# Performance work log

Hardware: AMD Instinct MI355X
Metric: run time of the kernel (lower is better)

## Reference

```python
import jax, jax.numpy as jnp
import numpy as np

NUM_HEADS = 16
ROPE_BASE = 10000.0
QK_GAIN_INIT = 12.0
EPS = 1e-6
# head_config = alternating ['rope','nope',...]; 1.0 -> RoPE applied to this head
ROPE_MASK = jnp.asarray(np.tile([1.0, 0.0], NUM_HEADS // 2), dtype=jnp.float32)


def setup_inputs() -> dict:
    key = jax.random.key(0)
    k0, k1, k2 = jax.random.split(key, 3)
    B, S, Dm = 2, 2048, 2048
    x = jax.random.normal(k0, (B, S, Dm), dtype=jnp.float32)
    # fused QKV projection and output projection (out_proj flagged zero-init in the
    # original; we use small random init so outputs/grads are non-trivial)
    w_qkv = jax.random.normal(k1, (Dm, 3 * Dm), dtype=jnp.float32) * (Dm ** -0.5)
    w_out = jax.random.normal(k2, (Dm, Dm), dtype=jnp.float32) * (Dm ** -0.5)
    q_gain = jnp.full((NUM_HEADS,), QK_GAIN_INIT, dtype=jnp.float32)
    return {"x": x, "w_qkv": w_qkv, "w_out": w_out, "q_gain": q_gain}


def _rope_cos_sin(seqlen, head_dim, dtype):
    half = head_dim // 2
    inv_freq = ROPE_BASE ** (-jnp.arange(0, half, dtype=jnp.float32) / half)
    theta = jnp.arange(seqlen, dtype=jnp.float32)[:, None] * inv_freq[None, :]  # [S, D/2]
    return jnp.cos(theta).astype(dtype), jnp.sin(theta).astype(dtype)


def _apply_rope(t, cos, sin):
    # t: [B, S, H, D]; cos/sin: [S, D/2] -> broadcast [1, S, 1, D/2]
    d2 = t.shape[-1] // 2
    t1, t2 = t[..., :d2], t[..., d2:]
    c = cos[None, :, None, :]
    s = sin[None, :, None, :]
    return jnp.concatenate([t1 * c - t2 * s, t1 * s + t2 * c], axis=-1)


def _unit_norm(t):
    # per-head-dim L2 normalization (qk-norm)
    return t * jax.lax.rsqrt(jnp.sum(t * t, axis=-1, keepdims=True) + EPS)


def reference(x, w_qkv, w_out, q_gain):
    B, S, Dm = x.shape
    H = NUM_HEADS
    D = Dm // H
    qkv = (x @ w_qkv).reshape(B, S, 3, H, D)
    q, k, v = qkv[:, :, 0], qkv[:, :, 1], qkv[:, :, 2]  # [B, S, H, D]
    q = _unit_norm(q)
    k = _unit_norm(k)
    cos, sin = _rope_cos_sin(S, D, x.dtype)
    m = ROPE_MASK[None, None, :, None]  # heterogeneous per-head dispatch
    q = m * _apply_rope(q, cos, sin) + (1.0 - m) * q
    k = m * _apply_rope(k, cos, sin) + (1.0 - m) * k
    # per-head learned qk gain instead of 1/sqrt(d)
    logits = jnp.einsum('bshd,bthd->bhst', q, k) * q_gain[None, :, None, None]
    causal = jnp.tril(jnp.ones((S, S), dtype=bool))
    logits = jnp.where(causal[None, None], logits, jnp.finfo(logits.dtype).min)
    attn = jax.nn.softmax(logits, axis=-1)
    y = jnp.einsum('bhst,bthd->bshd', attn, v).reshape(B, S, Dm)
    return y @ w_out
```

## Files before the change

### kernel.cpp

```cpp
#include <hip/hip_runtime.h>
#include <hip/hip_bf16.h>

typedef unsigned short ushort_t;
typedef __attribute__((ext_vector_type(8))) short short8;
typedef __attribute__((ext_vector_type(4))) float floatx4;

#define B_  2
#define S_  2048
#define DM_ 2048
#define H_  16
#define DH_ 128

#define AS1(p) ((const __attribute__((address_space(1))) void*)(p))
#define AS3(p) ((__attribute__((address_space(3))) void*)(p))

static __device__ __forceinline__ float b2f(ushort_t u) {
  __hip_bfloat16 h = *reinterpret_cast<__hip_bfloat16*>(&u);
  return __bfloat162float(h);
}
static __device__ __forceinline__ ushort_t f2b(float f) {
  __hip_bfloat16 h = __float2bfloat16(f);
  return *reinterpret_cast<ushort_t*>(&h);
}
static __device__ __forceinline__ float fast_exp2(float x) {
#if defined(__has_builtin)
#if __has_builtin(__builtin_amdgcn_exp2f)
  return __builtin_amdgcn_exp2f(x);
#else
  return exp2f(x);
#endif
#else
  return exp2f(x);
#endif
}

__global__ __launch_bounds__(256) void convert_f32_bf16(const float* __restrict__ in,
                                                        ushort_t* __restrict__ out) {
  size_t i = ((size_t)blockIdx.x * 256 + threadIdx.x) * 8;
  float4 a = *(const float4*)(in + i);
  float4 b = *(const float4*)(in + i + 4);
  ushort_t tmp[8] = {f2b(a.x), f2b(a.y), f2b(a.z), f2b(a.w),
                     f2b(b.x), f2b(b.y), f2b(b.z), f2b(b.w)};
  *(uint4*)(out + i) = *(const uint4*)tmp;
}

__global__ __launch_bounds__(256) void transpose_f32_to_bf16T(const float* __restrict__ in,
                                                              ushort_t* __restrict__ out,
                                                              int R, int inC, int colOff) {
  __shared__ ushort_t tile[64][72];
  const int tid = threadIdx.x;
  const int r0 = blockIdx.y * 64, c0 = blockIdx.x * 64;
#pragma unroll
  for (int p = 0; p < 2; ++p) {
    int li = tid + p * 256;
    int r = li >> 3, cs = (li & 7) * 8;
    const float* src = in + (size_t)(r0 + r) * inC + colOff + c0 + cs;
    float4 a = *(const float4*)src;
    float4 b = *(const float4*)(src + 4);
    ushort_t tmp[8] = {f2b(a.x), f2b(a.y), f2b(a.z), f2b(a.w),
                       f2b(b.x), f2b(b.y), f2b(b.z), f2b(b.w)};
    *(uint4*)&tile[r][cs] = *(const uint4*)tmp;
  }
  __syncthreads();
#pragma unroll
  for (int p = 0; p < 2; ++p) {
    int li = tid + p * 256;
    int cR = li >> 3, rs = (li & 7) * 8;
    ushort_t tmp[8];
#pragma unroll
    for (int e = 0; e < 8; ++e) tmp[e] = tile[rs + e][cR];
    *(uint4*)(out + (size_t)(c0 + cR) * R + r0 + rs) = *(const uint4*)tmp;
  }
}

template <int MODE>
__global__ __launch_bounds__(256) void gemm_bt_async(const ushort_t* __restrict__ A,
                                                     const ushort_t* __restrict__ Bt,
                                                     void* __restrict__ C0,
                                                     void* __restrict__ C1,
                                                     int M, int N, int K) {
  __shared__ alignas(16) ushort_t As[2][128 * 32];
  __shared__ alignas(16) ushort_t Bs[2][128 * 32];
  const int tid = threadIdx.x;
  const int wave = tid >> 6, lane = tid & 63;
  const int l15 = lane & 15, quad = lane >> 4;
  const int wr = (wave >> 1) * 64, wc = (wave & 1) * 64;
  const int lin = blockIdx.y * gridDim.x + blockIdx.x;
  const int band = lin / (4 * gridDim.x);
  const int rin = lin % (4 * gridDim.x);
  const int by = band * 4 + (rin & 3);
  const int bx = rin >> 2;
  const size_t m0 = (size_t)by * 128, n0 = (size_t)bx * 128;
  const int srow = lane >> 2, scol = (lane & 3) * 8;

  floatx4 zero = {0.f, 0.f, 0.f, 0.f};
  floatx4 acc[4][4];
#pragma unroll
  for (int i = 0; i < 4; ++i)
#pragma unroll
    for (int j = 0; j < 4; ++j) acc[i][j] = zero;

  auto stage = [&](int kt, int bf) {
#pragma unroll
    for (int i = 0; i < 2; ++i) {
      int c = wave * 2 + i;
      int row = c * 16 + srow;
      __builtin_amdgcn_global_load_lds(AS1(A + (m0 + row) * K + kt + scol),
                                       AS3((char*)As[bf] + c * 1024), 16, 0, 0);
      __builtin_amdgcn_global_load_lds(AS1(Bt + (n0 + row) * K + kt + scol),
                                       AS3((char*)Bs[bf] + c * 1024), 16, 0, 0);
    }
  };

  stage(0, 0);
  const int niter = K / 32;
  for (int it = 0; it < niter; ++it) {
    const int cur = it & 1;
    __syncthreads();
    if (it + 1 < niter) stage((it + 1) * 32, cur ^ 1);

    short8 af[4], bfr[4];
#pragma unroll
    for (int i = 0; i < 4; ++i)
      af[i] = *(const short8*)&As[cur][(wr + i * 16 + l15) * 32 + quad * 8];
#pragma unroll
    for (int j = 0; j < 4; ++j)
      bfr[j] = *(const short8*)&Bs[cur][(wc + j * 16 + l15) * 32 + quad * 8];
#pragma unroll
    for (int i = 0; i < 4; ++i)
#pragma unroll
      for (int j = 0; j < 4; ++j)
        acc[i][j] = __builtin_amdgcn_mfma_f32_16x16x32_bf16(af[i], bfr[j], acc[i][j], 0, 0, 0);
  }

#pragma unroll
  for (int i = 0; i < 4; ++i)
#pragma unroll
    for (int j = 0; j < 4; ++j)
#pragma unroll
      for (int r = 0; r < 4; ++r) {
        size_t row = m0 + wr + i * 16 + quad * 4 + r;
        size_t col = n0 + wc + j * 16 + l15;
        if (MODE == 1)
          ((float*)C0)[row * N + col] = acc[i][j][r];
        else
          ((ushort_t*)C0)[row * N + col] = f2b(acc[i][j][r]);
      }
}

#define SBAR() __builtin_amdgcn_sched_barrier(0)
#define BARR() __builtin_amdgcn_s_barrier()

#define LDS_A(qm, bb)                                                          \
  _Pragma("unroll") for (int mi = 0; mi < 4; ++mi) {                           \
    _Pragma("unroll") for (int ks = 0; ks < 2; ++ks) {                         \
      const int r_ = arow + (qm) * 64 + mi * 16;                               \
      const int cb_ = ((ks) * 64 + quad * 16) ^ swz;                           \
      afr[qm][mi][ks] =                                                        \
          *(const short8*)((const char*)As[bb] + r_ * 128 + cb_);              \
    }                                                                          \
  }

#define LDS_B(qn, bb)                                                          \
  _Pragma("unroll") for (int ni = 0; ni < 2; ++ni) {                           \
    _Pragma("unroll") for (int ks = 0; ks < 2; ++ks) {                         \
      const int r_ = brow + (qn) * 32 + ni * 16;                               \
      const int cb_ = ((ks) * 64 + quad * 16) ^ swz;                           \
      bfr[qn][ni][ks] =                                                        \
          *(const short8*)((const char*)Bs[bb] + r_ * 128 + cb_);              \
    }                                                                          \
  }

#define MMA_Q(qm, qn)                                                          \
  _Pragma("unroll") for (int mi = 0; mi < 4; ++mi) {                           \
    _Pragma("unroll") for (int ni = 0; ni < 2; ++ni) {                         \
      floatx4 t_ = acc[(qm) * 4 + mi][(qn) * 2 + ni];                          \
      t_ = __builtin_amdgcn_mfma_f32_16x16x32_bf16(afr[qm][mi][0],             \
                                                   bfr[qn][ni][0], t_, 0, 0, 0); \
      t_ = __builtin_amdgcn_mfma_f32_16x16x32_bf16(afr[qm][mi][1],             \
                                                   bfr[qn][ni][1], t_, 0, 0, 0); \
      acc[(qm) * 4 + mi][(qn) * 2 + ni] = t_;                                  \
    }                                                                          \
  }

template <int MODE>
__global__ __launch_bounds__(512, 2) void gemm_bt_256(const ushort_t* __restrict__ A,
                                                      const ushort_t* __restrict__ Bt,
                                                      void* __restrict__ C0,
                                                      void* __restrict__ C1,
                                                      int M, int N, int K) {
  __shared__ alignas(16) ushort_t As[2][256 * 64];
  __shared__ alignas(16) ushort_t Bs[2][256 * 64];
  const int tid = threadIdx.x;
  const int wave = tid >> 6, lane = tid & 63;
  const int l15 = lane & 15, quad = lane >> 4;
  const int wm = wave >> 2, wn = wave & 3;
  const size_t m0 = (size_t)blockIdx.y * 256, n0 = (size_t)blockIdx.x * 256;
  const int nkt = K >> 6;

  const int srow = lane >> 3;
  const int skk = ((lane & 7) ^ srow) * 8;

  const int arow = wm * 128 + l15;
  const int brow = wn * 64 + l15;
  const int swz = (l15 & 7) << 4;

  floatx4 zero = {0.f, 0.f, 0.f, 0.f};
  floatx4 acc[8][4];
#pragma unroll
  for (int i = 0; i < 8; ++i)
#pragma unroll
    for (int j = 0; j < 4; ++j) acc[i][j] = zero;

  short8 afr[2][4][2];
  short8 bfr[2][2][2];

  auto stage_half = [&](int t, int ht) {
    if (t >= nkt) return;
    const int bb = t & 1;
    const int h = ht & 1;
    const int kt64 = t << 6;
    const ushort_t* G = (ht < 2) ? A : Bt;
    const size_t r0 = (ht < 2) ? m0 : n0;
    char* dst = (char*)((ht < 2) ? As[bb] : Bs[bb]) + h * 16384;
#pragma unroll
    for (int i = 0; i < 2; ++i) {
      const int c = wave * 2 + i;
      const size_t gr = r0 + h * 128 + c * 8 + srow;
      __builtin_amdgcn_global_load_lds(AS1(G + gr * K + kt64 + skk),
                                       AS3(dst + c * 1024), 16, 0, 0);
    }
  };

  stage_half(0, 0); stage_half(0, 1); stage_half(0, 2); stage_half(0, 3);
  stage_half(1, 0); stage_half(1, 1); stage_half(1, 2); stage_half(1, 3);
  SBAR();
  if (nkt > 1) { asm volatile("s_waitcnt vmcnt(8)" ::: "memory"); }
  else         { asm volatile("s_waitcnt vmcnt(0)" ::: "memory"); }
  SBAR(); BARR(); SBAR();

  for (int kt = 0; kt < nkt; ++kt) {
    const int bb = kt & 1;
    LDS_A(0, bb); LDS_B(0, bb);
    SBAR(); BARR(); SBAR();
    __builtin_amdgcn_s_setprio(1);
    MMA_Q(0, 0);
    __builtin_amdgcn_s_setprio(0);
    SBAR(); BARR(); SBAR();
    LDS_A(1, bb);
    SBAR(); BARR(); SBAR();
    __builtin_amdgcn_s_setprio(1);
    MMA_Q(1, 0);
    __builtin_amdgcn_s_setprio(0);
    SBAR(); BARR(); SBAR();
    LDS_B(1, bb);
    stage_half(kt + 2, 0); stage_half(kt + 2, 1);
    SBAR(); BARR(); SBAR();
    __builtin_amdgcn_s_setprio(1);
    MMA_Q(1, 1);
    __builtin_amdgcn_s_setprio(0);
    SBAR(); BARR(); SBAR();
    stage_half(kt + 2, 2); stage_half(kt + 2, 3);
    SBAR(); BARR(); SBAR();
    __builtin_amdgcn_s_setprio(1);
    MMA_Q(0, 1);
    __builtin_amdgcn_s_setprio(0);
    SBAR();
    if (kt + 2 < nkt) { asm volatile("s_waitcnt vmcnt(8)" ::: "memory"); }
    else              { asm volatile("s_waitcnt vmcnt(0)" ::: "memory"); }
    SBAR(); BARR(); SBAR();
  }

  if (MODE == 2) {
    ushort_t* Cb = (n0 >= 2048) ? (ushort_t*)C1 : (ushort_t*)C0;
    size_t nc0 = n0 & 2047;
#pragma unroll
    for (int mi8 = 0; mi8 < 8; ++mi8)
#pragma unroll
      for (int nj = 0; nj < 4; ++nj)
#pragma unroll
        for (int r = 0; r < 4; ++r) {
          size_t row = m0 + wm * 128 + (mi8 >> 2) * 64 + (mi8 & 3) * 16 + quad * 4 + r;
          size_t col = nc0 + wn * 64 + (nj >> 1) * 32 + (nj & 1) * 16 + l15;
          Cb[row * 2048 + col] = f2b(acc[mi8][nj][r]);
        }
  } else {
#pragma unroll
    for (int mi8 = 0; mi8 < 8; ++mi8)
#pragma unroll
      for (int nj = 0; nj < 4; ++nj)
#pragma unroll
        for (int r = 0; r < 4; ++r) {
          size_t row = m0 + wm * 128 + (mi8 >> 2) * 64 + (mi8 & 3) * 16 + quad * 4 + r;
          size_t col = n0 + wn * 64 + (nj >> 1) * 32 + (nj & 1) * 16 + l15;
          if (MODE == 1)
            ((float*)C0)[row * N + col] = acc[mi8][nj][r];
          else
            ((ushort_t*)C0)[row * N + col] = f2b(acc[mi8][nj][r]);
        }
  }
}

__global__ __launch_bounds__(256) void norm_rope(ushort_t* __restrict__ Q,
                                                 ushort_t* __restrict__ Kb,
                                                 const float* __restrict__ gain) {
  const int tid = threadIdx.x;
  const int wave = tid >> 6, lane = tid & 63;
  const int g16 = lane >> 4, sl = lane & 15;
  const int idx = (blockIdx.x * 4 + wave) * 4 + g16;
  const int h = idx & 15;
  const int s = (idx >> 4) & (S_ - 1);
  const size_t off = (size_t)(idx >> 4) * DM_ + h * DH_ + sl * 4;

  ushort_t qv1[4], qv2[4], kv1[4], kv2[4];
  *(uint2*)qv1 = *(const uint2*)(Q + off);
  *(uint2*)qv2 = *(const uint2*)(Q + off + 64);
  *(uint2*)kv1 = *(const uint2*)(Kb + off);
  *(uint2*)kv2 = *(const uint2*)(Kb + off + 64);

  float q1[4], q2[4], k1[4], k2[4];
  float sq = 0.f, sk = 0.f;
#pragma unroll
  for (int e = 0; e < 4; ++e) {
    q1[e] = b2f(qv1[e]); q2[e] = b2f(qv2[e]);
    k1[e] = b2f(kv1[e]); k2[e] = b2f(kv2[e]);
    sq += q1[e] * q1[e] + q2[e] * q2[e];
    sk += k1[e] * k1[e] + k2[e] * k2[e];
  }
#pragma unroll
  for (int o = 1; o < 16; o <<= 1) {
    sq += __shfl_xor(sq, o, 64);
    sk += __shfl_xor(sk, o, 64);
  }
  float rq = rsqrtf(sq + 1e-6f), rk = rsqrtf(sk + 1e-6f);
  const float g = gain[h] * 1.44269504f;
  const bool roped = (h & 1) == 0;
#pragma unroll
  for (int e = 0; e < 4; ++e) {
    float a = q1[e] * rq, bq = q2[e] * rq;
    float c_ = k1[e] * rk, dk = k2[e] * rk;
    if (roped) {
      int j = sl * 4 + e;
      float invf = exp2f((float)j * -0.20762050593f);
      float th = (float)s * invf;
      float cc = cosf(th), sn = sinf(th);
      float na = a * cc - bq * sn, nb = a * sn + bq * cc;
      float nc = c_ * cc - dk * sn, nd = c_ * sn + dk * cc;
      a = na; bq = nb; c_ = nc; dk = nd;
    }
    qv1[e] = f2b(a * g); qv2[e] = f2b(bq * g);
    kv1[e] = f2b(c_);    kv2[e] = f2b(dk);
  }
  *(uint2*)(Q + off)       = *(const uint2*)qv1;
  *(uint2*)(Q + off + 64)  = *(const uint2*)qv2;
  *(uint2*)(Kb + off)      = *(const uint2*)kv1;
  *(uint2*)(Kb + off + 64) = *(const uint2*)kv2;
}

__global__ __launch_bounds__(256, 2) void attn(ushort_t* __restrict__ QY,
                                               const ushort_t* __restrict__ Kg,
                                               const ushort_t* __restrict__ Vg) {
  __shared__ alignas(16) ushort_t Ks[2][64 * 128];
  __shared__ alignas(16) ushort_t Vs[2][128 * 64];
  __shared__ alignas(16) ushort_t Ps[2][4][16 * 64];

  const float M0 = 18.755035531f;
  const int tid = threadIdx.x;
  const int wave = tid >> 6, lane = tid & 63;
  const int l15 = lane & 15, quad = lane >> 4;
  const int bh = blockIdx.x;
  const int b = bh >> 4, h = bh & 15;
  const int p = blockIdx.y;
  const int qt[2] = {p, 31 - p};

  const ushort_t* Kgb = Kg + (size_t)b * S_ * DM_ + h * DH_;
  const ushort_t* Vgb = Vg + (size_t)(h * DH_) * (B_ * S_) + b * S_;

  short8 aq[2][4];
#pragma unroll
  for (int t = 0; t < 2; ++t) {
    const ushort_t* Qg =
        QY + (size_t)(b * S_ + qt[t] * 64 + wave * 16 + l15) * DM_ + h * DH_;
#pragma unroll
    for (int ks = 0; ks < 4; ++ks)
      aq[t][ks] = *(const short8*)(Qg + ks * 32 + quad * 8);
  }

  float lsum[2][4] = {{0.f, 0.f, 0.f, 0.f}, {0.f, 0.f, 0.f, 0.f}};
  floatx4 zero = {0.f, 0.f, 0.f, 0.f};
  floatx4 oacc[2][8];
#pragma unroll
  for (int t = 0; t < 2; ++t)
#pragma unroll
    for (int d = 0; d < 8; ++d) oacc[t][d] = zero;

  const int krow_in = lane >> 4, ksd = lane & 15;
  const int vrow_in = lane >> 3, vsd = lane & 7;

  auto stage = [&](int kt, int bf) {
#pragma unroll
    for (int i = 0; i < 4; ++i) {
      int c = wave * 4 + i;
      {
        int r = c * 4 + krow_in;
        int sg = ksd ^ (r & 7);
        __builtin_amdgcn_global_load_lds(
            AS1(Kgb + (size_t)(kt * 64 + r) * DM_ + sg * 8),
            AS3((char*)Ks[bf] + c * 1024), 16, 0, 0);
      }
      {
        int r = c * 8 + vrow_in;
        int sg = vsd ^ (r & 7);
        __builtin_amdgcn_global_load_lds(
            AS1(Vgb + (size_t)r * (B_ * S_) + kt * 64 + sg * 8),
            AS3((char*)Vs[bf] + c * 1024), 16, 0, 0);
      }
    }
  };

  stage(0, 0);

  for (int kt = 0; kt <= qt[1]; ++kt) {
    const int cur = kt & 1;
    __syncthreads();
    if (kt < qt[1]) stage(kt + 1, cur ^ 1);

#pragma unroll
    for (int t = 0; t < 2; ++t) {
      if (t == 0 && kt > qt[0]) continue;
      floatx4 sacc[4];
#pragma unroll
      for (int j = 0; j < 4; ++j) sacc[j] = zero;
#pragma unroll
      for (int ks = 0; ks < 4; ++ks) {
#pragma unroll
        for (int j = 0; j < 4; ++j) {
          int row = j * 16 + l15;
          int sl = (ks * 4 + quad) ^ (row & 7);
          short8 bk = *(const short8*)&Ks[cur][row * 128 + sl * 8];
          sacc[j] = __builtin_amdgcn_mfma_f32_16x16x32_bf16(aq[t][ks], bk, sacc[j], 0, 0, 0);
        }
      }
      if (kt == qt[t]) {
#pragma unroll
        for (int j = 0; j < 4; ++j)
#pragma unroll
          for (int r = 0; r < 4; ++r) {
            int key = j * 16 + l15;
            int qr = wave * 16 + quad * 4 + r;
            if (key > qr) sacc[j][r] = -1e30f;
          }
      }
#pragma unroll
      for (int j = 0; j < 4; ++j)
#pragma unroll
        for (int r = 0; r < 4; ++r) {
          float pv = fast_exp2(sacc[j][r] - M0);
          sacc[j][r] = pv;
          lsum[t][r] += pv;
        }
#pragma unroll
      for (int j = 0; j < 4; ++j)
#pragma unroll
        for (int r = 0; r < 4; ++r) {
          int row = quad * 4 + r;
          int col = j * 16 + l15;
          int g = col >> 3, w = col & 7;
          Ps[t][wave][row * 64 + ((g ^ (row & 7)) << 3) + w] = f2b(sacc[j][r]);
        }
#pragma unroll
      for (int ks2 = 0; ks2 < 2; ++ks2) {
        short8 ap = *(const short8*)&Ps[t][wave][l15 * 64 +
                                                (((ks2 * 4 + quad) ^ (l15 & 7)) << 3)];
#pragma unroll
        for (int d = 0; d < 8; ++d) {
          int row = d * 16 + l15;
          int sl = (ks2 * 4 + quad) ^ (row & 7);
          short8 bv = *(const short8*)&Vs[cur][row * 64 + sl * 8];
          oacc[t][d] = __builtin_amdgcn_mfma_f32_16x16x32_bf16(ap, bv, oacc[t][d], 0, 0, 0);
        }
      }
    }
  }

#pragma unroll
  for (int t = 0; t < 2; ++t) {
#pragma unroll
    for (int r = 0; r < 4; ++r) {
#pragma unroll
      for (int o = 1; o < 16; o <<= 1) lsum[t][r] += __shfl_xor(lsum[t][r], o, 64);
      float inv = 1.0f / lsum[t][r];
      size_t row = (size_t)(b * S_ + qt[t] * 64 + wave * 16 + quad * 4 + r);
#pragma unroll
      for (int d = 0; d < 8; ++d) {
        size_t col = (size_t)h * DH_ + d * 16 + l15;
        QY[row * DM_ + col] = f2b(oacc[t][d][r] * inv);
      }
    }
  }
}

extern "C" void kernel_launch(void* const* d_in, const int* in_sizes, int n_in,
                              void* d_out, int out_size, void* d_ws, size_t ws_size,
                              hipStream_t stream) {
  const float* x      = (const float*)d_in[0];
  const float* w_qkv  = (const float*)d_in[1];
  const float* w_out  = (const float*)d_in[2];
  const float* q_gain = (const float*)d_in[3];
  float* out = (float*)d_out;

  char* ws = (char*)d_ws;
  const size_t bsd = (size_t)B_ * S_ * DM_;
  ushort_t* Qraw = (ushort_t*)ws;
  ushort_t* Kraw = Qraw + bsd;
  ushort_t* Vt   = Kraw + bsd;
  ushort_t* wvT  = Vt + bsd;
  ushort_t* xbf  = (ushort_t*)d_out;
  ushort_t* wqkT = xbf + bsd;
  ushort_t* woutT = Kraw;

  convert_f32_bf16<<<dim3(bsd / (8 * 256)), 256, 0, stream>>>(x, xbf);
  transpose_f32_to_bf16T<<<dim3(64, 32), 256, 0, stream>>>(w_qkv, wqkT, DM_, 3 * DM_, 0);
  transpose_f32_to_bf16T<<<dim3(32, 32), 256, 0, stream>>>(w_qkv, wvT, DM_, 3 * DM_, 2 * DM_);

  gemm_bt_256<2><<<dim3(16, 16), 512, 0, stream>>>(xbf, wqkT, Qraw, Kraw,
                                                   B_ * S_, 2 * DM_, DM_);
  gemm_bt_async<0><<<dim3(32, 16), 256, 0, stream>>>(wvT, xbf, Vt, nullptr,
                                                     DM_, B_ * S_, DM_);
  norm_rope<<<dim3(B_ * S_ * H_ / 16), 256, 0, stream>>>(Qraw, Kraw, q_gain);
  attn<<<dim3(B_ * H_, S_ / 128), 256, 0, stream>>>(Qraw, Kraw, Vt);
  transpose_f32_to_bf16T<<<dim3(32, 32), 256, 0, stream>>>(w_out, woutT, DM_, DM_, 0);
  gemm_bt_async<1><<<dim3(16, 32), 256, 0, stream>>>(Qraw, woutT, out, nullptr,
                                                     B_ * S_, DM_, DM_);
}
```

Measured before the change: 372.7 us.

## Replace simple 128x128 GEMM with swizzled, phase-pipelined kernel; rebalance 256 GEMM prefetch

Replaces the simple double-buffered 128x128 K=32 GEMM used for the V projection and output projection with a new K=64 kernel. The new kernel uses XOR-swizzled LDS, quarter-tile async loads interleaved between MFMA phases, barriers with setprio, and two blocks per CU. The existing 256 GEMM's prefetch schedule is also changed to issue loads one iteration ahead in smaller pieces, with a lower vmcnt wait threshold. The aim is to overlap global loads with MFMA work and cut LDS bank conflicts. The cost is more barriers per iteration, and the shallower in-flight load depth in the 256 GEMM could expose latency.

Result: faster. 363.8 us (-2.4%).

```diff
diff --git a/kernel.cpp b/kernel.cpp
--- a/kernel.cpp
+++ b/kernel.cpp
@@ -71,81 +71,6 @@
     for (int e = 0; e < 8; ++e) tmp[e] = tile[rs + e][cR];
     *(uint4*)(out + (size_t)(c0 + cR) * R + r0 + rs) = *(const uint4*)tmp;
   }
-}
-
-template <int MODE>
-__global__ __launch_bounds__(256) void gemm_bt_async(const ushort_t* __restrict__ A,
-                                                     const ushort_t* __restrict__ Bt,
-                                                     void* __restrict__ C0,
-                                                     void* __restrict__ C1,
-                                                     int M, int N, int K) {
-  __shared__ alignas(16) ushort_t As[2][128 * 32];
-  __shared__ alignas(16) ushort_t Bs[2][128 * 32];
-  const int tid = threadIdx.x;
-  const int wave = tid >> 6, lane = tid & 63;
-  const int l15 = lane & 15, quad = lane >> 4;
-  const int wr = (wave >> 1) * 64, wc = (wave & 1) * 64;
-  const int lin = blockIdx.y * gridDim.x + blockIdx.x;
-  const int band = lin / (4 * gridDim.x);
-  const int rin = lin % (4 * gridDim.x);
-  const int by = band * 4 + (rin & 3);
-  const int bx = rin >> 2;
-  const size_t m0 = (size_t)by * 128, n0 = (size_t)bx * 128;
-  const int srow = lane >> 2, scol = (lane & 3) * 8;
-
-  floatx4 zero = {0.f, 0.f, 0.f, 0.f};
-  floatx4 acc[4][4];
-#pragma unroll
-  for (int i = 0; i < 4; ++i)
-#pragma unroll
-    for (int j = 0; j < 4; ++j) acc[i][j] = zero;
-
-  auto stage = [&](int kt, int bf) {
-#pragma unroll
-    for (int i = 0; i < 2; ++i) {
-      int c = wave * 2 + i;
-      int row = c * 16 + srow;
-      __builtin_amdgcn_global_load_lds(AS1(A + (m0 + row) * K + kt + scol),
-                                       AS3((char*)As[bf] + c * 1024), 16, 0, 0);
-      __builtin_amdgcn_global_load_lds(AS1(Bt + (n0 + row) * K + kt + scol),
-                                       AS3((char*)Bs[bf] + c * 1024), 16, 0, 0);
-    }
-  };
-
-  stage(0, 0);
-  const int niter = K / 32;
-  for (int it = 0; it < niter; ++it) {
-    const int cur = it & 1;
-    __syncthreads();
-    if (it + 1 < niter) stage((it + 1) * 32, cur ^ 1);
-
-    short8 af[4], bfr[4];
-#pragma unroll
-    for (int i = 0; i < 4; ++i)
-      af[i] = *(const short8*)&As[cur][(wr + i * 16 + l15) * 32 + quad * 8];
-#pragma unroll
-    for (int j = 0; j < 4; ++j)
-      bfr[j] = *(const short8*)&Bs[cur][(wc + j * 16 + l15) * 32 + quad * 8];
-#pragma unroll
-    for (int i = 0; i < 4; ++i)
-#pragma unroll
-      for (int j = 0; j < 4; ++j)
-        acc[i][j] = __builtin_amdgcn_mfma_f32_16x16x32_bf16(af[i], bfr[j], acc[i][j], 0, 0, 0);
-  }
-
-#pragma unroll
-  for (int i = 0; i < 4; ++i)
-#pragma unroll
-    for (int j = 0; j < 4; ++j)
-#pragma unroll
-      for (int r = 0; r < 4; ++r) {
-        size_t row = m0 + wr + i * 16 + quad * 4 + r;
-        size_t col = n0 + wc + j * 16 + l15;
-        if (MODE == 1)
-          ((float*)C0)[row * N + col] = acc[i][j][r];
-        else
-          ((ushort_t*)C0)[row * N + col] = f2b(acc[i][j][r]);
-      }
 }
 
 #define SBAR() __builtin_amdgcn_sched_barrier(0)
@@ -233,40 +158,42 @@
   };
 
   stage_half(0, 0); stage_half(0, 1); stage_half(0, 2); stage_half(0, 3);
-  stage_half(1, 0); stage_half(1, 1); stage_half(1, 2); stage_half(1, 3);
+  stage_half(1, 0); stage_half(1, 1);
   SBAR();
-  if (nkt > 1) { asm volatile("s_waitcnt vmcnt(8)" ::: "memory"); }
+  if (nkt > 1) { asm volatile("s_waitcnt vmcnt(4)" ::: "memory"); }
   else         { asm volatile("s_waitcnt vmcnt(0)" ::: "memory"); }
   SBAR(); BARR(); SBAR();
 
   for (int kt = 0; kt < nkt; ++kt) {
     const int bb = kt & 1;
     LDS_A(0, bb); LDS_B(0, bb);
+    stage_half(kt + 1, 2);
     SBAR(); BARR(); SBAR();
     __builtin_amdgcn_s_setprio(1);
     MMA_Q(0, 0);
     __builtin_amdgcn_s_setprio(0);
     SBAR(); BARR(); SBAR();
     LDS_A(1, bb);
+    stage_half(kt + 1, 3);
     SBAR(); BARR(); SBAR();
     __builtin_amdgcn_s_setprio(1);
     MMA_Q(1, 0);
     __builtin_amdgcn_s_setprio(0);
     SBAR(); BARR(); SBAR();
     LDS_B(1, bb);
-    stage_half(kt + 2, 0); stage_half(kt + 2, 1);
+    stage_half(kt + 2, 0);
     SBAR(); BARR(); SBAR();
     __builtin_amdgcn_s_setprio(1);
     MMA_Q(1, 1);
     __builtin_amdgcn_s_setprio(0);
     SBAR(); BARR(); SBAR();
-    stage_half(kt + 2, 2); stage_half(kt + 2, 3);
+    stage_half(kt + 2, 1);
     SBAR(); BARR(); SBAR();
     __builtin_amdgcn_s_setprio(1);
     MMA_Q(0, 1);
     __builtin_amdgcn_s_setprio(0);
     SBAR();
-    if (kt + 2 < nkt) { asm volatile("s_waitcnt vmcnt(8)" ::: "memory"); }
+    if (kt + 2 < nkt) { asm volatile("s_waitcnt vmcnt(4)" ::: "memory"); }
     else              { asm volatile("s_waitcnt vmcnt(0)" ::: "memory"); }
     SBAR(); BARR(); SBAR();
   }
@@ -299,6 +226,147 @@
             ((ushort_t*)C0)[row * N + col] = f2b(acc[mi8][nj][r]);
         }
   }
+}
+
+#define LDS_A8(mh, bb)                                                         \
+  _Pragma("unroll") for (int mi = 0; mi < 2; ++mi) {                           \
+    _Pragma("unroll") for (int ks = 0; ks < 2; ++ks) {                         \
+      const int r_ = arow + ((mh) * 2 + mi) * 16;                              \
+      const int cb_ = ((ks) * 64 + quad * 16) ^ swz;                           \
+      afr[(mh) * 2 + mi][ks] =                                                 \
+          *(const short8*)((const char*)As[bb] + r_ * 128 + cb_);              \
+    }                                                                          \
+  }
+
+#define LDS_B8(nh, bb)                                                         \
+  _Pragma("unroll") for (int ni = 0; ni < 2; ++ni) {                           \
+    _Pragma("unroll") for (int ks = 0; ks < 2; ++ks) {                         \
+      const int r_ = brow + ((nh) * 2 + ni) * 16;                              \
+      const int cb_ = ((ks) * 64 + quad * 16) ^ swz;                           \
+      bfr[(nh) * 2 + ni][ks] =                                                 \
+          *(const short8*)((const char*)Bs[bb] + r_ * 128 + cb_);              \
+    }                                                                          \
+  }
+
+#define MMA_H(mh, nh)                                                          \
+  _Pragma("unroll") for (int mi = 0; mi < 2; ++mi) {                           \
+    _Pragma("unroll") for (int ni = 0; ni < 2; ++ni) {                         \
+      floatx4 t_ = acc[(mh) * 2 + mi][(nh) * 2 + ni];                          \
+      t_ = __builtin_amdgcn_mfma_f32_16x16x32_bf16(afr[(mh) * 2 + mi][0],      \
+                                                   bfr[(nh) * 2 + ni][0], t_, 0, 0, 0); \
+      t_ = __builtin_amdgcn_mfma_f32_16x16x32_bf16(afr[(mh) * 2 + mi][1],      \
+                                                   bfr[(nh) * 2 + ni][1], t_, 0, 0, 0); \
+      acc[(mh) * 2 + mi][(nh) * 2 + ni] = t_;                                  \
+    }                                                                          \
+  }
+
+template <int MODE>
+__global__ __launch_bounds__(256, 2) void gemm_bt_128(const ushort_t* __restrict__ A,
+                                                      const ushort_t* __restrict__ Bt,
+                                                      void* __restrict__ C0,
+                                                      int M, int N, int K) {
+  __shared__ alignas(16) ushort_t As[2][128 * 64];
+  __shared__ alignas(16) ushort_t Bs[2][128 * 64];
+  const int tid = threadIdx.x;
+  const int wave = tid >> 6, lane = tid & 63;
+  const int l15 = lane & 15, quad = lane >> 4;
+  const int wm = wave >> 1, wn = wave & 1;
+  const int lin = blockIdx.y * gridDim.x + blockIdx.x;
+  const int band = lin / (4 * gridDim.x);
+  const int rin = lin % (4 * gridDim.x);
+  const int by = band * 4 + (rin & 3);
+  const int bx = rin >> 2;
+  const size_t m0 = (size_t)by * 128, n0 = (size_t)bx * 128;
+  const int nkt = K >> 6;
+
+  const int srow = lane >> 3;
+  const int skk = ((lane & 7) ^ srow) * 8;
+
+  const int arow = wm * 64 + l15;
+  const int brow = wn * 64 + l15;
+  const int swz = (l15 & 7) << 4;
+
+  floatx4 zero = {0.f, 0.f, 0.f, 0.f};
+  floatx4 acc[4][4];
+#pragma unroll
+  for (int i = 0; i < 4; ++i)
+#pragma unroll
+    for (int j = 0; j < 4; ++j) acc[i][j] = zero;
+
+  short8 afr[4][2];
+  short8 bfr[4][2];
+
+  auto stage_q = [&](int t, int qt_) {
+    if (t >= nkt) return;
+    const int bb = t & 1;
+    const int h = qt_ & 1;
+    const int kt64 = t << 6;
+    const ushort_t* G = (qt_ < 2) ? A : Bt;
+    const size_t r0 = (qt_ < 2) ? m0 : n0;
+    char* dst = (char*)((qt_ < 2) ? As[bb] : Bs[bb]) + h * 8192;
+#pragma unroll
+    for (int i = 0; i < 2; ++i) {
+      const int c = wave * 2 + i;
+      const size_t gr = r0 + h * 64 + c * 8 + srow;
+      __builtin_amdgcn_global_load_lds(AS1(G + gr * K + kt64 + skk),
+                                       AS3(dst + c * 1024), 16, 0, 0);
+    }
+  };
+
+  stage_q(0, 0); stage_q(0, 1); stage_q(0, 2); stage_q(0, 3);
+  stage_q(1, 0); stage_q(1, 1);
+  SBAR();
+  if (nkt > 1) { asm volatile("s_waitcnt vmcnt(4)" ::: "memory"); }
+  else         { asm volatile("s_waitcnt vmcnt(0)" ::: "memory"); }
+  SBAR(); BARR(); SBAR();
+
+  for (int kt = 0; kt < nkt; ++kt) {
+    const int bb = kt & 1;
+    LDS_A8(0, bb); LDS_B8(0, bb);
+    stage_q(kt + 1, 2);
+    SBAR(); BARR(); SBAR();
+    __builtin_amdgcn_s_setprio(1);
+    MMA_H(0, 0);
+    __builtin_amdgcn_s_setprio(0);
+    SBAR(); BARR(); SBAR();
+    LDS_A8(1, bb);
+    stage_q(kt + 1, 3);
+    SBAR(); BARR(); SBAR();
+    __builtin_amdgcn_s_setprio(1);
+    MMA_H(1, 0);
+    __builtin_amdgcn_s_setprio(0);
+    SBAR(); BARR(); SBAR();
+    LDS_B8(1, bb);
+    stage_q(kt + 2, 0);
+    SBAR(); BARR(); SBAR();
+    __builtin_amdgcn_s_setprio(1);
+    MMA_H(1, 1);
+    __builtin_amdgcn_s_setprio(0);
+    SBAR(); BARR(); SBAR();
+    stage_q(kt + 2, 1);
+    SBAR(); BARR(); SBAR();
+    __builtin_amdgcn_s_setprio(1);
+    MMA_H(0, 1);
+    __builtin_amdgcn_s_setprio(0);
+    SBAR();
+    if (kt + 2 < nkt) { asm volatile("s_waitcnt vmcnt(4)" ::: "memory"); }
+    else              { asm volatile("s_waitcnt vmcnt(0)" ::: "memory"); }
+    SBAR(); BARR(); SBAR();
+  }
+
+#pragma unroll
+  for (int i = 0; i < 4; ++i)
+#pragma unroll
+    for (int j = 0; j < 4; ++j)
+#pragma unroll
+      for (int r = 0; r < 4; ++r) {
+        size_t row = m0 + wm * 64 + i * 16 + quad * 4 + r;
+        size_t col = n0 + wn * 64 + j * 16 + l15;
+        if (MODE == 1)
+          ((float*)C0)[row * N + col] = acc[i][j][r];
+        else
+          ((ushort_t*)C0)[row * N + col] = f2b(acc[i][j][r]);
+      }
 }
 
 __global__ __launch_bounds__(256) void norm_rope(ushort_t* __restrict__ Q,
@@ -525,11 +593,11 @@
 
   gemm_bt_256<2><<<dim3(16, 16), 512, 0, stream>>>(xbf, wqkT, Qraw, Kraw,
                                                    B_ * S_, 2 * DM_, DM_);
-  gemm_bt_async<0><<<dim3(32, 16), 256, 0, stream>>>(wvT, xbf, Vt, nullptr,
-                                                     DM_, B_ * S_, DM_);
+  gemm_bt_128<0><<<dim3(32, 16), 256, 0, stream>>>(wvT, xbf, Vt,
+                                                   DM_, B_ * S_, DM_);
   norm_rope<<<dim3(B_ * S_ * H_ / 16), 256, 0, stream>>>(Qraw, Kraw, q_gain);
   attn<<<dim3(B_ * H_, S_ / 128), 256, 0, stream>>>(Qraw, Kraw, Vt);
   transpose_f32_to_bf16T<<<dim3(32, 32), 256, 0, stream>>>(w_out, woutT, DM_, DM_, 0);
-  gemm_bt_async<1><<<dim3(16, 32), 256, 0, stream>>>(Qraw, woutT, out, nullptr,
-                                                     B_ * S_, DM_, DM_);
-}
+  gemm_bt_128<1><<<dim3(16, 32), 256, 0, stream>>>(Qraw, woutT, out,
+                                                   B_ * S_, DM_, DM_);
+}
```
